# Performance work log

Hardware: AMD Instinct MI355X
Metric: run time of the kernel (lower is better)

## Reference

```python
import jax, jax.numpy as jnp
import numpy as np


def _gcn_norm(edge_index, num_nodes, dtype):
    # PyG GCNConv.norm: add self-loops (weight 1), symmetric deg^{-1/2} normalization
    row, col = edge_index[0], edge_index[1]
    loop = jnp.arange(num_nodes, dtype=row.dtype)
    row = jnp.concatenate([row, loop])
    col = jnp.concatenate([col, loop])
    ew = jnp.ones(row.shape[0], dtype=dtype)
    deg = jax.ops.segment_sum(ew, row, num_segments=num_nodes)
    dis = jnp.where(deg > 0, jax.lax.rsqrt(deg), 0.0)
    norm = dis[row] * ew * dis[col]
    return row, col, norm


def _masked_gcn_conv(x, row, col, norm, sigma, W, b, num_nodes):
    # mask_features: edge gather -> diff/sigma -> square -> scatter-add -> exp mask
    h = (x[col] - x[row]) / sigma            # [E, F]
    h = norm[:, None] * h * h                # [E, F]
    mask = jax.ops.segment_sum(h, row, num_segments=num_nodes)        # [N, F]
    deg = jax.ops.segment_sum(jnp.ones_like(norm), row, num_segments=num_nodes)  # degree(source), >=1 due to self-loops
    x = x * jnp.exp(-mask / deg[:, None])
    # GCNConv: linear transform then normalized aggregation source->target
    xw = x @ W                               # [N, O]
    out = jax.ops.segment_sum(norm[:, None] * xw[row], col, num_segments=num_nodes)
    return out + b


def setup_inputs() -> dict:
    key = jax.random.key(0)
    ks = jax.random.split(key, 8)
    N, E, F, H, C = 100000, 1600000, 128, 64, 40
    g = 1.414  # xavier gain used for sigma
    return {
        "x": jax.random.normal(ks[0], (N, F), jnp.float32),
        "edge_index": jax.random.randint(ks[1], (2, E), 0, N, jnp.int64),
        "sigma1": jax.random.uniform(ks[2], (1, F), jnp.float32, -1.0, 1.0) * (g * np.sqrt(6.0 / (1 + F))),
        "W1": jax.random.normal(ks[3], (F, H), jnp.float32) * (1.0 / np.sqrt(F)),
        "b1": jnp.zeros((H,), jnp.float32),
        "sigma2": jax.random.uniform(ks[4], (1, H), jnp.float32, -1.0, 1.0) * (g * np.sqrt(6.0 / (1 + H))),
        "W2": jax.random.normal(ks[5], (H, C), jnp.float32) * (1.0 / np.sqrt(H)),
        "b2": jnp.zeros((C,), jnp.float32),
    }


def reference(x, edge_index, sigma1, W1, b1, sigma2, W2, b2):
    N = x.shape[0]
    row, col, norm = _gcn_norm(edge_index, N, x.dtype)
    x = _masked_gcn_conv(x, row, col, norm, sigma1, W1, b1, N)
    x = jax.nn.relu(x)
    # dropout is identity in eval mode
    x = _masked_gcn_conv(x, row, col, norm, sigma2, W2, b2, N)
    return jax.nn.log_softmax(x, axis=1)
```

## Files before the change

### kernel.cpp

```cpp
#include <hip/hip_runtime.h>
#include <cmath>

constexpr int F1 = 128;
constexpr int H  = 64;
constexpr int NC = 40;
constexpr int NCOPY = 8;

constexpr int SCAN_TPB = 256;
constexpr int SCAN_IPT = 8;
constexpr int SCAN_EPB = SCAN_TPB * SCAN_IPT;

__device__ inline unsigned short f2bf(float f) {
    union { float f; unsigned u; } v; v.f = f;
    return (unsigned short)((v.u + 0x7FFFu + ((v.u >> 16) & 1u)) >> 16);
}
__device__ inline float bflo(unsigned p) { union { float f; unsigned u; } v; v.u = p << 16; return v.f; }
__device__ inline float bfhi(unsigned p) { union { float f; unsigned u; } v; v.u = p & 0xFFFF0000u; return v.f; }
__device__ inline void unpack8(uint4 raw, float* d) {
    d[0] = bflo(raw.x); d[1] = bfhi(raw.x); d[2] = bflo(raw.y); d[3] = bfhi(raw.y);
    d[4] = bflo(raw.z); d[5] = bfhi(raw.z); d[6] = bflo(raw.w); d[7] = bfhi(raw.w);
}

__global__ void isg_kernel(const float* __restrict__ s1, float* __restrict__ i1,
                           const float* __restrict__ s2, float* __restrict__ i2) {
    int i = threadIdx.x;
    if (i < F1) i1[i] = 1.0f / s1[i];
    if (i < H)  i2[i] = 1.0f / s2[i];
}

__global__ void count1_prep_kernel(const int* __restrict__ row, const int* __restrict__ col,
                                   int* __restrict__ cnt8, int E, int N, int cntBlocks,
                                   const float* __restrict__ x, const float* __restrict__ isg,
                                   unsigned short* __restrict__ u, size_t n8) {
    int bid = blockIdx.x;
    if (bid < cntBlocks) {
        int e = bid * 256 + threadIdx.x;
        if (e < E) {
            int* cnt = cnt8 + (size_t)(bid & (NCOPY - 1)) * 2 * N;
            atomicAdd(&cnt[row[e]], 1);
            atomicAdd(&cnt[N + col[e]], 1);
        }
    } else {
        size_t idx = (size_t)(bid - cntBlocks) * 256 + threadIdx.x;
        if (idx >= n8) return;
        size_t base = idx * 8;
        int fk = (int)(base % (size_t)F1);
        float4 a0 = *(const float4*)&x[base];
        float4 a1 = *(const float4*)&x[base + 4];
        float4 s0 = *(const float4*)&isg[fk];
        float4 s1 = *(const float4*)&isg[fk + 4];
        uint4 p4;
        p4.x = (unsigned)f2bf(a0.x * s0.x) | ((unsigned)f2bf(a0.y * s0.y) << 16);
        p4.y = (unsigned)f2bf(a0.z * s0.z) | ((unsigned)f2bf(a0.w * s0.w) << 16);
        p4.z = (unsigned)f2bf(a1.x * s1.x) | ((unsigned)f2bf(a1.y * s1.y) << 16);
        p4.w = (unsigned)f2bf(a1.z * s1.z) | ((unsigned)f2bf(a1.w * s1.w) << 16);
        *(uint4*)&u[base] = p4;
    }
}

__global__ void scan_partial_kernel(const int* __restrict__ cnt8, int* __restrict__ bsum, int M) {
    __shared__ int red[SCAN_TPB];
    int t = threadIdx.x;
    int i0 = blockIdx.x * SCAN_EPB + t * SCAN_IPT;
    int s = 0;
#pragma unroll
    for (int k = 0; k < SCAN_IPT; ++k) {
        int i = i0 + k;
        if (i < M) {
#pragma unroll
            for (int c = 0; c < NCOPY; ++c) s += cnt8[(size_t)c * M + i];
        }
    }
    red[t] = s;
    __syncthreads();
    for (int off = SCAN_TPB / 2; off > 0; off >>= 1) {
        if (t < off) red[t] += red[t + off];
        __syncthreads();
    }
    if (t == 0) bsum[blockIdx.x] = red[0];
}

__global__ void scan_offsets_kernel(int* __restrict__ bsum, int nb,
                                    int* __restrict__ rowptrO, int* __restrict__ rowptrI,
                                    int N, int E) {
    __shared__ int sh[1024];
    int t = threadIdx.x;
    sh[t] = (t < nb) ? bsum[t] : 0;
    __syncthreads();
    for (int off = 1; off < 1024; off <<= 1) {
        int v = (t >= off) ? sh[t - off] : 0;
        __syncthreads();
        sh[t] += v;
        __syncthreads();
    }
    if (t < nb) bsum[t] = (t > 0) ? sh[t - 1] : 0;
    if (t == 0) { rowptrO[N] = E; rowptrI[N] = E; }
}

__global__ void scan_final_kernel(const int* __restrict__ cnt8, int* __restrict__ cur8,
                                  const int* __restrict__ bsum,
                                  int* __restrict__ rowptrO, int* __restrict__ rowptrI,
                                  float* __restrict__ dis, int N, int E) {
    __shared__ int sh[SCAN_TPB];
    int t = threadIdx.x;
    int M = 2 * N;
    int i0 = blockIdx.x * SCAN_EPB + t * SCAN_IPT;
    int tot[SCAN_IPT], pre[SCAN_IPT];
    int run = 0;
#pragma unroll
    for (int k = 0; k < SCAN_IPT; ++k) {
        int i = i0 + k;
        int s = 0;
        if (i < M) {
#pragma unroll
            for (int c = 0; c < NCOPY; ++c) s += cnt8[(size_t)c * M + i];
        }
        tot[k] = s;
        pre[k] = run;
        run += s;
    }
    sh[t] = run;
    __syncthreads();
    for (int off = 1; off < SCAN_TPB; off <<= 1) {
        int v = (t >= off) ? sh[t - off] : 0;
        __syncthreads();
        sh[t] += v;
        __syncthreads();
    }
    int toff = ((t > 0) ? sh[t - 1] : 0) + bsum[blockIdx.x];
#pragma unroll
    for (int k = 0; k < SCAN_IPT; ++k) {
        int i = i0 + k;
        if (i < M) {
            int val = toff + pre[k];
            int base;
            if (i < N) {
                rowptrO[i] = val;
                dis[i] = rsqrtf((float)(tot[k] + 1));
                base = val;
            } else {
                rowptrI[i - N] = val - E;
                base = val - E;
            }
            int b = base;
#pragma unroll
            for (int c = 0; c < NCOPY; ++c) {
                cur8[(size_t)c * M + i] = b;
                b += cnt8[(size_t)c * M + i];
            }
        }
    }
}

__global__ void build1_kernel(const int* __restrict__ row, const int* __restrict__ col,
                              int* __restrict__ cur8,
                              int2* __restrict__ adjO2, int2* __restrict__ adjI2,
                              const float* __restrict__ dis, int E, int N) {
    int bid = blockIdx.x;
    int e = bid * 256 + threadIdx.x;
    if (e >= E) return;
    int* cur = cur8 + (size_t)(bid & (NCOPY - 1)) * 2 * N;
    int r = row[e], c = col[e];
    float nrm = dis[r] * dis[c];
    int nb = __float_as_int(nrm);
    adjO2[atomicAdd(&cur[r], 1)] = make_int2(c, nb);
    adjI2[atomicAdd(&cur[N + c], 1)] = make_int2(r, nb);
}

template<int F, int O, int R>
__global__ void fused_mask_gemm_kernel(const int* __restrict__ rowptr, const int2* __restrict__ adj2,
                                       const float* __restrict__ sig,
                                       const unsigned short* __restrict__ u,
                                       const float* __restrict__ W,
                                       unsigned short* __restrict__ Ybf, int N) {
    constexpr int NT = R * 64;
    constexpr int G = F / 8;
    constexpr int NPI = 64 / G;
    __shared__ __align__(16) float Ws[F * O];
    __shared__ __align__(16) float Xs[R][F];
    int tid = threadIdx.x;
    for (int i = tid; i < F * O; i += NT) Ws[i] = W[i];
    int w = tid >> 6, lane = tid & 63;
    int h = lane / G, j = lane % G;
    int base = blockIdx.x * R;
    int r = base + w;
    if (r < N) {
        int beg = rowptr[r], end = rowptr[r + 1];
        float inv_deg = 1.0f / (float)(end - beg + 1);
        float ur[8], acc[8];
        unpack8(*(const uint4*)&u[(size_t)r * F + 8 * j], ur);
#pragma unroll
        for (int k = 0; k < 8; ++k) acc[k] = 0.0f;
        for (int t = beg; t < end; t += 2 * NPI) {
            int e0 = t + h, e1 = t + NPI + h;
            int2 a0 = adj2[min(e0, end - 1)];
            int2 a1 = adj2[min(e1, end - 1)];
            float n0 = (e0 < end) ? __int_as_float(a0.y) : 0.0f;
            float n1 = (e1 < end) ? __int_as_float(a1.y) : 0.0f;
            uint4 rw0 = *(const uint4*)&u[(size_t)a0.x * F + 8 * j];
            uint4 rw1 = *(const uint4*)&u[(size_t)a1.x * F + 8 * j];
            float uc[8];
            unpack8(rw0, uc);
#pragma unroll
            for (int q = 0; q < 8; ++q) {
                float d = uc[q] - ur[q];
                acc[q] = fmaf(n0 * d, d, acc[q]);
            }
            unpack8(rw1, uc);
#pragma unroll
            for (int q = 0; q < 8; ++q) {
                float d = uc[q] - ur[q];
                acc[q] = fmaf(n1 * d, d, acc[q]);
            }
        }
#pragma unroll
        for (int off = G; off < 64; off <<= 1) {
#pragma unroll
            for (int k = 0; k < 8; ++k) acc[k] += __shfl_xor(acc[k], off);
        }
        if (h == 0) {
            float4 s0 = *(const float4*)&sig[8 * j];
            float4 s1 = *(const float4*)&sig[8 * j + 4];
            float sg[8] = {s0.x, s0.y, s0.z, s0.w, s1.x, s1.y, s1.z, s1.w};
            float xm[8];
#pragma unroll
            for (int k = 0; k < 8; ++k) xm[k] = ur[k] * sg[k] * expf(-acc[k] * inv_deg);
            *(float4*)&Xs[w][8 * j]     = make_float4(xm[0], xm[1], xm[2], xm[3]);
            *(float4*)&Xs[w][8 * j + 4] = make_float4(xm[4], xm[5], xm[6], xm[7]);
        }
    } else if (h == 0) {
        *(float4*)&Xs[w][8 * j]     = make_float4(0.f, 0.f, 0.f, 0.f);
        *(float4*)&Xs[w][8 * j + 4] = make_float4(0.f, 0.f, 0.f, 0.f);
    }
    __syncthreads();
    if (w < 2) {
        int r0 = base + 4 * w;
        if (r0 < N && lane < O) {
            float a0 = 0.f, a1 = 0.f, a2 = 0.f, a3 = 0.f;
#pragma unroll
            for (int fq = 0; fq < F / 4; ++fq) {
                float4 x0 = *(const float4*)&Xs[4 * w + 0][4 * fq];
                float4 x1 = *(const float4*)&Xs[4 * w + 1][4 * fq];
                float4 x2 = *(const float4*)&Xs[4 * w + 2][4 * fq];
                float4 x3 = *(const float4*)&Xs[4 * w + 3][4 * fq];
                float w0 = Ws[(4 * fq + 0) * O + lane];
                float w1 = Ws[(4 * fq + 1) * O + lane];
                float w2 = Ws[(4 * fq + 2) * O + lane];
                float w3 = Ws[(4 * fq + 3) * O + lane];
                a0 = fmaf(x0.x, w0, a0); a0 = fmaf(x0.y, w1, a0); a0 = fmaf(x0.z, w2, a0); a0 = fmaf(x0.w, w3, a0);
                a1 = fmaf(x1.x, w0, a1); a1 = fmaf(x1.y, w1, a1); a1 = fmaf(x1.z, w2, a1); a1 = fmaf(x1.w, w3, a1);
                a2 = fmaf(x2.x, w0, a2); a2 = fmaf(x2.y, w1, a2); a2 = fmaf(x2.z, w2, a2); a2 = fmaf(x2.w, w3, a2);
                a3 = fmaf(x3.x, w0, a3); a3 = fmaf(x3.y, w1, a3); a3 = fmaf(x3.z, w2, a3); a3 = fmaf(x3.w, w3, a3);
            }
            float o0 = __shfl_xor(a0, 1);
            float o1 = __shfl_xor(a1, 1);
            float o2 = __shfl_xor(a2, 1);
            float o3 = __shfl_xor(a3, 1);
            if (!(lane & 1)) {
                *(unsigned*)&Ybf[(size_t)r0 * O + lane] = (unsigned)f2bf(a0) | ((unsigned)f2bf(o0) << 16);
                if (r0 + 1 < N) *(unsigned*)&Ybf[(size_t)(r0 + 1) * O + lane] = (unsigned)f2bf(a1) | ((unsigned)f2bf(o1) << 16);
                if (r0 + 2 < N) *(unsigned*)&Ybf[(size_t)(r0 + 2) * O + lane] = (unsigned)f2bf(a2) | ((unsigned)f2bf(o2) << 16);
                if (r0 + 3 < N) *(unsigned*)&Ybf[(size_t)(r0 + 3) * O + lane] = (unsigned)f2bf(a3) | ((unsigned)f2bf(o3) << 16);
            }
        }
    }
}

__global__ void agg_relu_kernel(const int* __restrict__ rowptr, const int2* __restrict__ adj2,
                                const float* __restrict__ dis, const unsigned short* __restrict__ ybf,
                                const float* __restrict__ bias,
                                unsigned short* __restrict__ u2, const float* __restrict__ isg2, int N) {
    int c = blockIdx.x * (blockDim.x >> 6) + (threadIdx.x >> 6);
    if (c >= N) return;
    int lane = threadIdx.x & 63;
    int h = lane >> 3, j = lane & 7;
    int beg = rowptr[c], end = rowptr[c + 1];
    float acc[8];
#pragma unroll
    for (int k = 0; k < 8; ++k) acc[k] = 0.0f;
    for (int t = beg; t < end; t += 16) {
        int e0 = t + h, e1 = t + 8 + h;
        int2 a0 = adj2[min(e0, end - 1)];
        int2 a1 = adj2[min(e1, end - 1)];
        float n0 = (e0 < end) ? __int_as_float(a0.y) : 0.0f;
        float n1 = (e1 < end) ? __int_as_float(a1.y) : 0.0f;
        uint4 rw0 = *(const uint4*)&ybf[(size_t)a0.x * H + 8 * j];
        uint4 rw1 = *(const uint4*)&ybf[(size_t)a1.x * H + 8 * j];
        float v[8];
        unpack8(rw0, v);
#pragma unroll
        for (int q = 0; q < 8; ++q) acc[q] = fmaf(n0, v[q], acc[q]);
        unpack8(rw1, v);
#pragma unroll
        for (int q = 0; q < 8; ++q) acc[q] = fmaf(n1, v[q], acc[q]);
    }
#pragma unroll
    for (int off = 8; off < 64; off <<= 1) {
#pragma unroll
        for (int k = 0; k < 8; ++k) acc[k] += __shfl_xor(acc[k], off);
    }
    if (h == 0) {
        float dc = dis[c];
        float sv[8];
        unpack8(*(const uint4*)&ybf[(size_t)c * H + 8 * j], sv);
        float4 b0 = *(const float4*)&bias[8 * j];
        float4 b1v = *(const float4*)&bias[8 * j + 4];
        float bb[8] = {b0.x, b0.y, b0.z, b0.w, b1v.x, b1v.y, b1v.z, b1v.w};
        float4 s0 = *(const float4*)&isg2[8 * j];
        float4 s1 = *(const float4*)&isg2[8 * j + 4];
        float sg[8] = {s0.x, s0.y, s0.z, s0.w, s1.x, s1.y, s1.z, s1.w};
        float hv[8];
        float d2 = dc * dc;
#pragma unroll
        for (int k = 0; k < 8; ++k) hv[k] = fmaxf(fmaf(d2, sv[k], acc[k]) + bb[k], 0.0f);
        uint4 p;
        p.x = (unsigned)f2bf(hv[0] * sg[0]) | ((unsigned)f2bf(hv[1] * sg[1]) << 16);
        p.y = (unsigned)f2bf(hv[2] * sg[2]) | ((unsigned)f2bf(hv[3] * sg[3]) << 16);
        p.z = (unsigned)f2bf(hv[4] * sg[4]) | ((unsigned)f2bf(hv[5] * sg[5]) << 16);
        p.w = (unsigned)f2bf(hv[6] * sg[6]) | ((unsigned)f2bf(hv[7] * sg[7]) << 16);
        *(uint4*)&u2[(size_t)c * H + 8 * j] = p;
    }
}

__global__ void agg_lsm_kernel(const int* __restrict__ rowptr, const int2* __restrict__ adj2,
                               const float* __restrict__ dis, const unsigned short* __restrict__ ybf,
                               const float* __restrict__ bias, float* __restrict__ out, int N) {
    int c = blockIdx.x * (blockDim.x >> 6) + (threadIdx.x >> 6);
    if (c >= N) return;
    int lane = threadIdx.x & 63;
    int h = lane >> 4, j = lane & 15;
    bool active = j < 10;
    int beg = rowptr[c], end = rowptr[c + 1];
    float a[4] = {0.f, 0.f, 0.f, 0.f};
    for (int t = beg; t < end; t += 8) {
        int e0 = t + h, e1 = t + 4 + h;
        int2 a0 = adj2[min(e0, end - 1)];
        int2 a1 = adj2[min(e1, end - 1)];
        float n0 = (e0 < end) ? __int_as_float(a0.y) : 0.0f;
        float n1 = (e1 < end) ? __int_as_float(a1.y) : 0.0f;
        uint2 rw0 = active ? *(const uint2*)&ybf[(size_t)a0.x * NC + 4 * j] : make_uint2(0u, 0u);
        uint2 rw1 = active ? *(const uint2*)&ybf[(size_t)a1.x * NC + 4 * j] : make_uint2(0u, 0u);
        a[0] = fmaf(n0, bflo(rw0.x), a[0]); a[1] = fmaf(n0, bfhi(rw0.x), a[1]);
        a[2] = fmaf(n0, bflo(rw0.y), a[2]); a[3] = fmaf(n0, bfhi(rw0.y), a[3]);
        a[0] = fmaf(n1, bflo(rw1.x), a[0]); a[1] = fmaf(n1, bfhi(rw1.x), a[1]);
        a[2] = fmaf(n1, bflo(rw1.y), a[2]); a[3] = fmaf(n1, bfhi(rw1.y), a[3]);
    }
#pragma unroll
    for (int off = 16; off < 64; off <<= 1) {
#pragma unroll
        for (int k = 0; k < 4; ++k) a[k] += __shfl_xor(a[k], off);
    }
    bool wr = (h == 0) && active;
    float v[4] = {-INFINITY, -INFINITY, -INFINITY, -INFINITY};
    if (wr) {
        float dc = dis[c];
        uint2 sr = *(const uint2*)&ybf[(size_t)c * NC + 4 * j];
        float sv[4] = {bflo(sr.x), bfhi(sr.x), bflo(sr.y), bfhi(sr.y)};
        float4 bb = *(const float4*)&bias[4 * j];
        float b4[4] = {bb.x, bb.y, bb.z, bb.w};
        float d2 = dc * dc;
#pragma unroll
        for (int k = 0; k < 4; ++k) v[k] = fmaf(d2, sv[k], a[k]) + b4[k];
    }
    float m = fmaxf(fmaxf(v[0], v[1]), fmaxf(v[2], v[3]));
#pragma unroll
    for (int off = 8; off > 0; off >>= 1) m = fmaxf(m, __shfl_xor(m, off));
    float s = wr ? (expf(v[0] - m) + expf(v[1] - m) + expf(v[2] - m) + expf(v[3] - m)) : 0.0f;
#pragma unroll
    for (int off = 8; off > 0; off >>= 1) s += __shfl_xor(s, off);
    float mls = m + logf(s);
    if (wr)
        *(float4*)&out[(size_t)c * NC + 4 * j] = make_float4(v[0] - mls, v[1] - mls, v[2] - mls, v[3] - mls);
}

extern "C" void kernel_launch(void* const* d_in, const int* in_sizes, int n_in,
                              void* d_out, int out_size, void* d_ws, size_t ws_size,
                              hipStream_t stream) {
    const float* x    = (const float*)d_in[0];
    const int*   ei   = (const int*)  d_in[1];
    const float* sig1 = (const float*)d_in[2];
    const float* W1   = (const float*)d_in[3];
    const float* b1   = (const float*)d_in[4];
    const float* sig2 = (const float*)d_in[5];
    const float* W2   = (const float*)d_in[6];
    const float* b2   = (const float*)d_in[7];
    float* out = (float*)d_out;

    const int N = in_sizes[0] / F1;
    const int E = in_sizes[1] / 2;
    const int* row = ei;
    const int* col = ei + E;

    char* w = (char*)d_ws;
    auto alloc = [&](size_t bytes) { void* q = w; w += (bytes + 255) & ~255ull; return q; };
    int*   rowptrO = (int*)  alloc((size_t)(N + 1) * 4);
    int*   rowptrI = (int*)  alloc((size_t)(N + 1) * 4);
    int2*  adjO2   = (int2*) alloc((size_t)E * 8);
    int2*  adjI2   = (int2*) alloc((size_t)E * 8);
    float* dis     = (float*)alloc((size_t)N * 4);
    float* isg1    = (float*)alloc(F1 * 4);
    float* isg2    = (float*)alloc(H * 4);
    int*   bsum    = (int*)  alloc(1024 * 4);
    unsigned short* u1   = (unsigned short*)alloc((size_t)N * F1 * 2);
    unsigned short* u2   = (unsigned short*)alloc((size_t)N * H * 2);
    unsigned short* ybf1 = (unsigned short*)alloc((size_t)N * H * 2);
    unsigned short* ybf2 = u1;
    int* cnt8 = (int*)u2;
    int* cur8 = (int*)ybf1;

    const int B = 256;
    const int cntBlocks = (E + B - 1) / B;
    const size_t n8 = (size_t)N * F1 / 8;
    const int prepBlocks = (int)((n8 + B - 1) / B);
    const int M = 2 * N;
    const int nb = (M + SCAN_EPB - 1) / SCAN_EPB;

    hipMemsetAsync(cnt8, 0, (size_t)NCOPY * M * 4, stream);
    isg_kernel<<<1, 128, 0, stream>>>(sig1, isg1, sig2, isg2);
    count1_prep_kernel<<<cntBlocks + prepBlocks, B, 0, stream>>>(
        row, col, cnt8, E, N, cntBlocks, x, isg1, u1, n8);
    scan_partial_kernel<<<nb, SCAN_TPB, 0, stream>>>(cnt8, bsum, M);
    scan_offsets_kernel<<<1, 1024, 0, stream>>>(bsum, nb, rowptrO, rowptrI, N, E);
    scan_final_kernel<<<nb, SCAN_TPB, 0, stream>>>(cnt8, cur8, bsum, rowptrO, rowptrI, dis, N, E);
    build1_kernel<<<cntBlocks, B, 0, stream>>>(row, col, cur8, adjO2, adjI2, dis, E, N);

    fused_mask_gemm_kernel<F1, H, 8><<<(N + 7) / 8, 512, 0, stream>>>(rowptrO, adjO2, sig1, u1, W1, ybf1, N);
    agg_relu_kernel<<<(N + 3) / 4, B, 0, stream>>>(rowptrI, adjI2, dis, ybf1, b1, u2, isg2, N);

    fused_mask_gemm_kernel<H, NC, 8><<<(N + 7) / 8, 512, 0, stream>>>(rowptrO, adjO2, sig2, u2, W2, ybf2, N);
    agg_lsm_kernel<<<(N + 3) / 4, B, 0, stream>>>(rowptrI, adjI2, dis, ybf2, b2, out, N);
}
```

Measured before the change: 694.5 us.

## Partition CSR build by node range instead of replicated cursor copies

Replaces the per-block replicated cursor arrays (8 copies) used during CSR fill with a single cursor array and a build kernel where each block group owns one-eighth of the node range. Every group scans all edges and only scatters edges whose row or column falls in its partition, so atomics and writes stay within a smaller region that fits better in cache. The cost is reading the edge list eight times, and the cursor setup in the scan kernel gets simpler.

```diff
diff --git a/kernel.cpp b/kernel.cpp
--- a/kernel.cpp
+++ b/kernel.cpp
@@ -4,6 +4,7 @@
 constexpr int F1 = 128;
 constexpr int H  = 64;
 constexpr int NC = 40;
+constexpr int NPART = 8;
 constexpr int NCOPY = 8;
 
 constexpr int SCAN_TPB = 256;
@@ -97,7 +98,8 @@
     if (t == 0) { rowptrO[N] = E; rowptrI[N] = E; }
 }
 
-__global__ void scan_final_kernel(const int* __restrict__ cnt8, int* __restrict__ cur8,
+__global__ void scan_final_kernel(const int* __restrict__ cnt8,
+                                  int* __restrict__ curO, int* __restrict__ curI,
                                   const int* __restrict__ bsum,
                                   int* __restrict__ rowptrO, int* __restrict__ rowptrI,
                                   float* __restrict__ dis, int N, int E) {
@@ -133,38 +135,37 @@
         int i = i0 + k;
         if (i < M) {
             int val = toff + pre[k];
-            int base;
             if (i < N) {
                 rowptrO[i] = val;
+                curO[i] = val;
                 dis[i] = rsqrtf((float)(tot[k] + 1));
-                base = val;
             } else {
                 rowptrI[i - N] = val - E;
-                base = val - E;
+                curI[i - N] = val - E;
             }
-            int b = base;
-#pragma unroll
-            for (int c = 0; c < NCOPY; ++c) {
-                cur8[(size_t)c * M + i] = b;
-                b += cnt8[(size_t)c * M + i];
-            }
-        }
-    }
-}
-
-__global__ void build1_kernel(const int* __restrict__ row, const int* __restrict__ col,
-                              int* __restrict__ cur8,
+        }
+    }
+}
+
+__global__ void build8_kernel(const int* __restrict__ row, const int* __restrict__ col,
+                              int* __restrict__ curO, int* __restrict__ curI,
                               int2* __restrict__ adjO2, int2* __restrict__ adjI2,
-                              const float* __restrict__ dis, int E, int N) {
-    int bid = blockIdx.x;
-    int e = bid * 256 + threadIdx.x;
-    if (e >= E) return;
-    int* cur = cur8 + (size_t)(bid & (NCOPY - 1)) * 2 * N;
-    int r = row[e], c = col[e];
-    float nrm = dis[r] * dis[c];
-    int nb = __float_as_int(nrm);
-    adjO2[atomicAdd(&cur[r], 1)] = make_int2(c, nb);
-    adjI2[atomicAdd(&cur[N + c], 1)] = make_int2(r, nb);
+                              const float* __restrict__ dis,
+                              int E, int chunk, int stride) {
+    int p = blockIdx.x & (NPART - 1);
+    int gid = blockIdx.x / NPART;
+    unsigned lo = (unsigned)(p * chunk);
+    for (int e = gid * blockDim.x + threadIdx.x; e < E; e += stride) {
+        int r = row[e], c = col[e];
+        bool inR = (unsigned)r - lo < (unsigned)chunk;
+        bool inC = (unsigned)c - lo < (unsigned)chunk;
+        if (inR | inC) {
+            float nrm = dis[r] * dis[c];
+            int nb = __float_as_int(nrm);
+            if (inR) adjO2[atomicAdd(&curO[r], 1)] = make_int2(c, nb);
+            if (inC) adjI2[atomicAdd(&curI[c], 1)] = make_int2(r, nb);
+        }
+    }
 }
 
 template<int F, int O, int R>
@@ -393,6 +394,8 @@
 
     char* w = (char*)d_ws;
     auto alloc = [&](size_t bytes) { void* q = w; w += (bytes + 255) & ~255ull; return q; };
+    int*   curO    = (int*)  alloc((size_t)2 * N * 4);
+    int*   curI    = curO + N;
     int*   rowptrO = (int*)  alloc((size_t)(N + 1) * 4);
     int*   rowptrI = (int*)  alloc((size_t)(N + 1) * 4);
     int2*  adjO2   = (int2*) alloc((size_t)E * 8);
@@ -406,9 +409,11 @@
     unsigned short* ybf1 = (unsigned short*)alloc((size_t)N * H * 2);
     unsigned short* ybf2 = u1;
     int* cnt8 = (int*)u2;
-    int* cur8 = (int*)ybf1;
 
     const int B = 256;
+    const int chunk = (N + NPART - 1) / NPART;
+    const int TOTB = 8192;
+    const int stride8 = (TOTB / NPART) * B;
     const int cntBlocks = (E + B - 1) / B;
     const size_t n8 = (size_t)N * F1 / 8;
     const int prepBlocks = (int)((n8 + B - 1) / B);
@@ -421,8 +426,8 @@
         row, col, cnt8, E, N, cntBlocks, x, isg1, u1, n8);
     scan_partial_kernel<<<nb, SCAN_TPB, 0, stream>>>(cnt8, bsum, M);
     scan_offsets_kernel<<<1, 1024, 0, stream>>>(bsum, nb, rowptrO, rowptrI, N, E);
-    scan_final_kernel<<<nb, SCAN_TPB, 0, stream>>>(cnt8, cur8, bsum, rowptrO, rowptrI, dis, N, E);
-    build1_kernel<<<cntBlocks, B, 0, stream>>>(row, col, cur8, adjO2, adjI2, dis, E, N);
+    scan_final_kernel<<<nb, SCAN_TPB, 0, stream>>>(cnt8, curO, curI, bsum, rowptrO, rowptrI, dis, N, E);
+    build8_kernel<<<TOTB, B, 0, stream>>>(row, col, curO, curI, adjO2, adjI2, dis, E, chunk, stride8);
 
     fused_mask_gemm_kernel<F1, H, 8><<<(N + 7) / 8, 512, 0, stream>>>(rowptrO, adjO2, sig1, u1, W1, ybf1, N);
     agg_relu_kernel<<<(N + 3) / 4, B, 0, stream>>>(rowptrI, adjI2, dis, ybf1, b1, u2, isg2, N);
```

Result: faster. 616.7 us (-11.2%).
